# Kernel optimization log

Measured on AMD Instinct MI355X. Metric: run time of the kernel, lower is better.

The kernel has to match this reference:

```python
import jax, jax.numpy as jnp
import numpy as np

VOCAB = 50257
H = 1024
T = 4096


def setup_inputs() -> dict:
    key = jax.random.key(0)
    ks = jax.random.split(key, 6)
    scale = 1.0 / np.sqrt(H)  # matches torch LSTM uniform(-1/sqrt(H), 1/sqrt(H)) scale
    return {
        "tokens": jax.random.randint(ks[0], (T,), 0, VOCAB),
        "emb": jax.random.normal(ks[1], (VOCAB, H), dtype=jnp.float32) * 0.02,
        "w_ih": jax.random.uniform(ks[2], (4 * H, H), jnp.float32, -scale, scale),
        "w_hh": jax.random.uniform(ks[3], (4 * H, H), jnp.float32, -scale, scale),
        "b_ih": jax.random.uniform(ks[4], (4 * H,), jnp.float32, -scale, scale),
        "b_hh": jax.random.uniform(ks[5], (4 * H,), jnp.float32, -scale, scale),
    }


def _lstm(x, w_ih, w_hh, b_ih, b_hh):
    # x: [T, H]. Precompute input-side gate projections for all timesteps.
    gx = x @ w_ih.T + (b_ih + b_hh)  # [T, 4H]

    def step(carry, g_t):
        h, c = carry  # [H], [H]
        gates = g_t + h @ w_hh.T  # [4H]
        i, f, g, o = jnp.split(gates, 4)  # torch gate order: input, forget, cell, output
        i = jax.nn.sigmoid(i)
        f = jax.nn.sigmoid(f)
        g = jnp.tanh(g)
        o = jax.nn.sigmoid(o)
        c = f * c + i * g
        h = o * jnp.tanh(c)
        return (h, c), h

    h0 = jnp.zeros((H,), x.dtype)
    c0 = jnp.zeros((H,), x.dtype)
    (h_f, c_f), hs = jax.lax.scan(step, (h0, c0), gx)
    return hs, h_f, c_f  # hs: [T, H]


def reference(tokens, emb, w_ih, w_hh, b_ih, b_hh):
    x = emb[tokens]  # [T, H] embedding lookup
    hs, h_f, c_f = _lstm(x, w_ih, w_hh, b_ih, b_hh)
    output = hs[None, :, :]          # [1, T, H]  (batch_first, batch=1)
    h_n = h_f[None, None, :]         # [1, 1, H]
    c_n = c_f[None, None, :]         # [1, 1, H]
    return (output, (h_n, c_n))
```

## Files before the change

### kernel.cpp

```cpp
#include <hip/hip_runtime.h>
#include <hip/hip_bf16.h>

#define HD   1024
#define GD   4096
#define TT   4096
#define NWG  256

#define BM 128
#define BN 128
#define BK 16
#define LDP 132

__global__ __launch_bounds__(256, 2) void gemm_gx(
    const int* __restrict__ tokens,
    const float* __restrict__ emb,
    const float* __restrict__ Wih,
    const float* __restrict__ bih,
    const float* __restrict__ bhh,
    float* __restrict__ gxout)
{
    __shared__ float As[BK][LDP];
    __shared__ float Bs[BK][LDP];
    const int tid = threadIdx.x;
    const int m0 = blockIdx.x * BM;
    const int n0 = blockIdx.y * BN;
    const int tx = tid & 15;
    const int ty = tid >> 4;

    const int quad = tid & 3;
    const int r0   = tid >> 2;
    const int tok0 = tokens[m0 + r0];
    const int tok1 = tokens[m0 + r0 + 64];

    float acc[8][8] = {};

    for (int kt = 0; kt < HD; kt += BK) {
        float4 av0 = *reinterpret_cast<const float4*>(
            &emb[(size_t)tok0 * HD + kt + quad * 4]);
        float4 bv0 = *reinterpret_cast<const float4*>(
            &Wih[(size_t)(n0 + r0) * HD + kt + quad * 4]);
        float4 av1 = *reinterpret_cast<const float4*>(
            &emb[(size_t)tok1 * HD + kt + quad * 4]);
        float4 bv1 = *reinterpret_cast<const float4*>(
            &Wih[(size_t)(n0 + r0 + 64) * HD + kt + quad * 4]);
        As[quad * 4 + 0][r0] = av0.x;
        As[quad * 4 + 1][r0] = av0.y;
        As[quad * 4 + 2][r0] = av0.z;
        As[quad * 4 + 3][r0] = av0.w;
        Bs[quad * 4 + 0][r0] = bv0.x;
        Bs[quad * 4 + 1][r0] = bv0.y;
        Bs[quad * 4 + 2][r0] = bv0.z;
        Bs[quad * 4 + 3][r0] = bv0.w;
        As[quad * 4 + 0][r0 + 64] = av1.x;
        As[quad * 4 + 1][r0 + 64] = av1.y;
        As[quad * 4 + 2][r0 + 64] = av1.z;
        As[quad * 4 + 3][r0 + 64] = av1.w;
        Bs[quad * 4 + 0][r0 + 64] = bv1.x;
        Bs[quad * 4 + 1][r0 + 64] = bv1.y;
        Bs[quad * 4 + 2][r0 + 64] = bv1.z;
        Bs[quad * 4 + 3][r0 + 64] = bv1.w;
        __syncthreads();
#pragma unroll
        for (int k = 0; k < BK; ++k) {
            float4 a0 = *reinterpret_cast<const float4*>(&As[k][ty * 8]);
            float4 a1 = *reinterpret_cast<const float4*>(&As[k][ty * 8 + 4]);
            float4 b0 = *reinterpret_cast<const float4*>(&Bs[k][tx * 8]);
            float4 b1 = *reinterpret_cast<const float4*>(&Bs[k][tx * 8 + 4]);
            float a[8] = {a0.x, a0.y, a0.z, a0.w, a1.x, a1.y, a1.z, a1.w};
            float b[8] = {b0.x, b0.y, b0.z, b0.w, b1.x, b1.y, b1.z, b1.w};
#pragma unroll
            for (int i = 0; i < 8; ++i)
#pragma unroll
                for (int j = 0; j < 8; ++j)
                    acc[i][j] += a[i] * b[j];
        }
        __syncthreads();
    }

    float bias[8];
#pragma unroll
    for (int j = 0; j < 8; ++j) {
        int n = n0 + tx * 8 + j;
        bias[j] = bih[n] + bhh[n];
    }
#pragma unroll
    for (int i = 0; i < 8; ++i) {
        size_t o = (size_t)(m0 + ty * 8 + i) * GD + n0 + tx * 8;
        float4 s0 = {acc[i][0] + bias[0], acc[i][1] + bias[1],
                     acc[i][2] + bias[2], acc[i][3] + bias[3]};
        float4 s1 = {acc[i][4] + bias[4], acc[i][5] + bias[5],
                     acc[i][6] + bias[6], acc[i][7] + bias[7]};
        *reinterpret_cast<float4*>(&gxout[o]) = s0;
        *reinterpret_cast<float4*>(&gxout[o + 4]) = s1;
    }
}

__device__ __forceinline__ float sigmoid_(float x) {
    return 1.f / (1.f + __expf(-x));
}
__device__ __forceinline__ float tanh_(float x) {
    return __builtin_fmaf(2.f, 1.f / (1.f + __expf(-2.f * x)), -1.f);
}
__device__ __forceinline__ float bcast_(float v, int l) {
    return __uint_as_float(__builtin_amdgcn_readlane(__float_as_uint(v), l));
}
__device__ __forceinline__ void lds_barrier_() {
    asm volatile("s_waitcnt lgkmcnt(0)" ::: "memory");
    __builtin_amdgcn_s_barrier();
}

using u32x4 = __attribute__((ext_vector_type(4))) unsigned int;

__global__ __launch_bounds__(256, 1) void lstm_scan(
    const float* __restrict__ gx,
    const float* __restrict__ whh,
    float* __restrict__ out,
    unsigned long long* __restrict__ hbuf)
{
    const int tid   = threadIdx.x;
    const int b     = blockIdx.x;
    const int lane  = tid & 63;
    const int wv    = tid >> 6;
    const int chunk = lane & 15;
    const int gate  = lane >> 4;
    const int j     = b * 4 + wv;
    const int R     = gate * HD + j;

    float w[64];
    {
        const float* wrow = whh + (size_t)R * HD;
#pragma unroll
        for (int q = 0; q < 16; ++q) {
            float4 v = *reinterpret_cast<const float4*>(&wrow[chunk * 4 + q * 64]);
            w[q * 4 + 0] = v.x; w[q * 4 + 1] = v.y;
            w[q * 4 + 2] = v.z; w[q * 4 + 3] = v.w;
        }
    }

    __shared__ float h_lds[2][HD];
#pragma unroll
    for (int q = 0; q < 4; ++q) h_lds[0][tid * 4 + q] = 0.f;
    lds_barrier_();

    float c_reg = 0.f;
    float gx_cur = gx[R];

    const int tp = (tid + b) & 255;
    unsigned long long* const pb0 = hbuf + (size_t)tp * 4;
    unsigned long long* const pb1 = hbuf + HD + (size_t)tp * 4;

    for (int s = 1; s <= TT; ++s) {
        const int cb = (s - 1) & 1;
        const int nb = s & 1;

        float gx_nxt = 0.f;
        if (s < TT) gx_nxt = gx[(size_t)s * GD + R];

        float A0 = (chunk == 0) ? gx_cur : 0.f;
        float A1 = 0.f, A2 = 0.f, A3 = 0.f;
        {
            const float* hb = h_lds[cb];
#pragma unroll
            for (int q = 0; q < 4; ++q) {
                float4 h0 = *reinterpret_cast<const float4*>(&hb[chunk * 4 + (4 * q + 0) * 64]);
                float4 h1 = *reinterpret_cast<const float4*>(&hb[chunk * 4 + (4 * q + 1) * 64]);
                float4 h2 = *reinterpret_cast<const float4*>(&hb[chunk * 4 + (4 * q + 2) * 64]);
                float4 h3 = *reinterpret_cast<const float4*>(&hb[chunk * 4 + (4 * q + 3) * 64]);
                A0 = __builtin_fmaf(w[(4 * q + 0) * 4 + 0], h0.x, A0);
                A0 = __builtin_fmaf(w[(4 * q + 0) * 4 + 1], h0.y, A0);
                A0 = __builtin_fmaf(w[(4 * q + 0) * 4 + 2], h0.z, A0);
                A0 = __builtin_fmaf(w[(4 * q + 0) * 4 + 3], h0.w, A0);
                A1 = __builtin_fmaf(w[(4 * q + 1) * 4 + 0], h1.x, A1);
                A1 = __builtin_fmaf(w[(4 * q + 1) * 4 + 1], h1.y, A1);
                A1 = __builtin_fmaf(w[(4 * q + 1) * 4 + 2], h1.z, A1);
                A1 = __builtin_fmaf(w[(4 * q + 1) * 4 + 3], h1.w, A1);
                A2 = __builtin_fmaf(w[(4 * q + 2) * 4 + 0], h2.x, A2);
                A2 = __builtin_fmaf(w[(4 * q + 2) * 4 + 1], h2.y, A2);
                A2 = __builtin_fmaf(w[(4 * q + 2) * 4 + 2], h2.z, A2);
                A2 = __builtin_fmaf(w[(4 * q + 2) * 4 + 3], h2.w, A2);
                A3 = __builtin_fmaf(w[(4 * q + 3) * 4 + 0], h3.x, A3);
                A3 = __builtin_fmaf(w[(4 * q + 3) * 4 + 1], h3.y, A3);
                A3 = __builtin_fmaf(w[(4 * q + 3) * 4 + 2], h3.z, A3);
                A3 = __builtin_fmaf(w[(4 * q + 3) * 4 + 3], h3.w, A3);
            }
        }
        float acc = (A0 + A1) + (A2 + A3);
        acc += __shfl_xor(acc, 1, 64);
        acc += __shfl_xor(acc, 2, 64);
        acc += __shfl_xor(acc, 4, 64);
        acc += __shfl_xor(acc, 8, 64);
        float si = bcast_(acc, 0);
        float sf = bcast_(acc, 16);
        float sg = bcast_(acc, 32);
        float so = bcast_(acc, 48);

        float ii = sigmoid_(si);
        float ff = sigmoid_(sf);
        float gg = tanh_(sg);
        float oo = sigmoid_(so);
        c_reg = __builtin_fmaf(ff, c_reg, ii * gg);
        float hh = oo * tanh_(c_reg);

        if (s < TT) {
            if (lane == 0) {
                unsigned long long pkt =
                    ((unsigned long long)(unsigned)s << 32) | __float_as_uint(hh);
                __hip_atomic_store(&hbuf[(size_t)nb * HD + j], pkt,
                                   __ATOMIC_RELAXED, __HIP_MEMORY_SCOPE_AGENT);
            }
            gx_cur = gx_nxt;

            if (tid != 0) {
                const unsigned int us = (unsigned int)s;
                unsigned long long* src = nb ? pb1 : pb0;
                u32x4 q0, q1;
                int r = 0;
                for (;;) {
                    asm volatile(
                        "global_load_dwordx4 %0, %2, off sc1\n\t"
                        "global_load_dwordx4 %1, %2, off offset:16 sc1\n\t"
                        "s_waitcnt vmcnt(0)"
                        : "=v"(q0), "=v"(q1)
                        : "v"(src)
                        : "memory");
                    bool ok = (q0.y == us) & (q0.w == us) &
                              (q1.y == us) & (q1.w == us);
                    if (ok) break;
                    ++r;
                    if (r > (1 << 17)) break;
                    if (r >= 6) __builtin_amdgcn_s_sleep(1);
                }
                float4 hv;
                hv.x = __uint_as_float(q0.x);
                hv.y = __uint_as_float(q0.z);
                hv.z = __uint_as_float(q1.x);
                hv.w = __uint_as_float(q1.z);
                *reinterpret_cast<float4*>(&h_lds[nb][tp * 4]) = hv;
            }
            if (lane == 0) {
                h_lds[nb][j] = hh;
                out[(size_t)(s - 1) * HD + j] = hh;
            }
            lds_barrier_();
        } else {
            if (lane == 0) {
                out[(size_t)(s - 1) * HD + j] = hh;
                out[(size_t)TT * HD + j] = hh;
                out[(size_t)TT * HD + HD + j] = c_reg;
            }
        }
    }
}

extern "C" void kernel_launch(void* const* d_in, const int* in_sizes, int n_in,
                              void* d_out, int out_size, void* d_ws, size_t ws_size,
                              hipStream_t stream) {
    const int*   tokens = (const int*)d_in[0];
    const float* emb    = (const float*)d_in[1];
    const float* w_ih   = (const float*)d_in[2];
    const float* w_hh   = (const float*)d_in[3];
    const float* b_ih   = (const float*)d_in[4];
    const float* b_hh   = (const float*)d_in[5];
    float* out = (float*)d_out;

    char* ws = (char*)d_ws;
    const size_t HBUF_BYTES = (size_t)2 * HD * 8;
    unsigned long long* hbuf = (unsigned long long*)ws;
    float* gx = (float*)(ws + 65536);

    hipMemsetAsync(hbuf, 0, HBUF_BYTES, stream);
    gemm_gx<<<dim3(TT / BM, GD / BN), 256, 0, stream>>>(tokens, emb, w_ih,
                                                        b_ih, b_hh, gx);
    lstm_scan<<<NWG, 256, 0, stream>>>(gx, w_hh, out, hbuf);
}
```

Measured before the change: 18.78 ms.

## Replicate LSTM scan per XCD with XCD-local mailboxes for h exchange

```diff
diff --git a/kernel.cpp b/kernel.cpp
--- a/kernel.cpp
+++ b/kernel.cpp
@@ -5,6 +5,8 @@
 #define GD   4096
 #define TT   4096
 #define NWG  256
+
+using u32x4 = __attribute__((ext_vector_type(4))) unsigned int;
 
 #define BM 128
 #define BN 128
@@ -101,154 +103,209 @@
 __device__ __forceinline__ float tanh_(float x) {
     return __builtin_fmaf(2.f, 1.f / (1.f + __expf(-2.f * x)), -1.f);
 }
-__device__ __forceinline__ float bcast_(float v, int l) {
-    return __uint_as_float(__builtin_amdgcn_readlane(__float_as_uint(v), l));
-}
 __device__ __forceinline__ void lds_barrier_() {
     asm volatile("s_waitcnt lgkmcnt(0)" ::: "memory");
     __builtin_amdgcn_s_barrier();
 }
-
-using u32x4 = __attribute__((ext_vector_type(4))) unsigned int;
-
-__global__ __launch_bounds__(256, 1) void lstm_scan(
+__device__ __forceinline__ float rl_(float v, int l) {
+    return __uint_as_float(__builtin_amdgcn_readlane(__float_as_uint(v), l));
+}
+__device__ __forceinline__ float dot4_(float4 a, float4 b, float c) {
+    c = __builtin_fmaf(a.x, b.x, c);
+    c = __builtin_fmaf(a.y, b.y, c);
+    c = __builtin_fmaf(a.z, b.z, c);
+    return __builtin_fmaf(a.w, b.w, c);
+}
+
+__global__ __launch_bounds__(512, 1) void lstm_scan(
     const float* __restrict__ gx,
     const float* __restrict__ whh,
     float* __restrict__ out,
-    unsigned long long* __restrict__ hbuf)
+    unsigned long long* __restrict__ mbF,
+    unsigned long long* __restrict__ mbS,
+    int* __restrict__ ctr)
 {
-    const int tid   = threadIdx.x;
-    const int b     = blockIdx.x;
-    const int lane  = tid & 63;
-    const int wv    = tid >> 6;
+    const int tid  = threadIdx.x;
+    const int lane = tid & 63;
+    const int wv   = tid >> 6;
+    const int sub  = lane >> 4;
     const int chunk = lane & 15;
-    const int gate  = lane >> 4;
-    const int j     = b * 4 + wv;
-    const int R     = gate * HD + j;
-
-    float w[64];
-    {
-        const float* wrow = whh + (size_t)R * HD;
-#pragma unroll
-        for (int q = 0; q < 16; ++q) {
-            float4 v = *reinterpret_cast<const float4*>(&wrow[chunk * 4 + q * 64]);
-            w[q * 4 + 0] = v.x; w[q * 4 + 1] = v.y;
-            w[q * 4 + 2] = v.z; w[q * 4 + 3] = v.w;
-        }
-    }
-
+
+    __shared__ int s_role, s_xcd, s_fail;
+    __shared__ float wlds[8][16][256];
     __shared__ float h_lds[2][HD];
-#pragma unroll
-    for (int q = 0; q < 4; ++q) h_lds[0][tid * 4 + q] = 0.f;
+
+    if (tid == 0) {
+        unsigned int x;
+        asm volatile("s_getreg_b32 %0, hwreg(20, 0, 32)" : "=s"(x));
+        x &= 7;
+        s_xcd  = (int)x;
+        s_role = atomicAdd(&ctr[x], 1);
+        s_fail = 0;
+    }
+    __syncthreads();
+    const int role = s_role;
+    if (role >= 32) return;
+
+    unsigned long long* const fastb = mbF + (size_t)s_xcd * 2048;
+    unsigned long long* const slowb = mbS + (size_t)s_xcd * 2048;
+    const int j0 = role * 32 + wv * 4;
+
+    float4 wreg[16][3];
+#pragma unroll
+    for (int rr = 0; rr < 16; ++rr) {
+        const float* wr = whh + (size_t)((rr >> 2) * HD + j0 + (rr & 3)) * HD;
+#pragma unroll
+        for (int q = 0; q < 3; ++q)
+            wreg[rr][q] = *reinterpret_cast<const float4*>(&wr[4 * lane + 256 * q]);
+        *reinterpret_cast<float4*>(&wlds[wv][rr][4 * lane]) =
+            *reinterpret_cast<const float4*>(&wr[4 * lane + 768]);
+    }
+
+    *reinterpret_cast<float2*>(&h_lds[0][2 * tid]) = float2{0.f, 0.f};
     lds_barrier_();
 
-    float c_reg = 0.f;
-    float gx_cur = gx[R];
-
-    const int tp = (tid + b) & 255;
-    unsigned long long* const pb0 = hbuf + (size_t)tp * 4;
-    unsigned long long* const pb1 = hbuf + HD + (size_t)tp * 4;
+    const int grow = (lane >> 2) * HD + j0 + (lane & 3);
+    float gxc = (lane < 16) ? gx[grow] : 0.f;
+
+    float cst[4] = {0.f, 0.f, 0.f, 0.f};
+    bool slow = false;
+    const int e0 = 2 * tid;
 
     for (int s = 1; s <= TT; ++s) {
         const int cb = (s - 1) & 1;
         const int nb = s & 1;
 
-        float gx_nxt = 0.f;
-        if (s < TT) gx_nxt = gx[(size_t)s * GD + R];
-
-        float A0 = (chunk == 0) ? gx_cur : 0.f;
-        float A1 = 0.f, A2 = 0.f, A3 = 0.f;
+        float gxn = 0.f;
+        if (s < TT && lane < 16) gxn = gx[(size_t)s * GD + grow];
+
+        float4 hq0 = *reinterpret_cast<const float4*>(&h_lds[cb][4 * lane]);
+        float4 hq1 = *reinterpret_cast<const float4*>(&h_lds[cb][4 * lane + 256]);
+        float4 hq2 = *reinterpret_cast<const float4*>(&h_lds[cb][4 * lane + 512]);
+        float4 hq3 = *reinterpret_cast<const float4*>(&h_lds[cb][4 * lane + 768]);
+
+        float ii[4], hh[4];
         {
-            const float* hb = h_lds[cb];
-#pragma unroll
-            for (int q = 0; q < 4; ++q) {
-                float4 h0 = *reinterpret_cast<const float4*>(&hb[chunk * 4 + (4 * q + 0) * 64]);
-                float4 h1 = *reinterpret_cast<const float4*>(&hb[chunk * 4 + (4 * q + 1) * 64]);
-                float4 h2 = *reinterpret_cast<const float4*>(&hb[chunk * 4 + (4 * q + 2) * 64]);
-                float4 h3 = *reinterpret_cast<const float4*>(&hb[chunk * 4 + (4 * q + 3) * 64]);
-                A0 = __builtin_fmaf(w[(4 * q + 0) * 4 + 0], h0.x, A0);
-                A0 = __builtin_fmaf(w[(4 * q + 0) * 4 + 1], h0.y, A0);
-                A0 = __builtin_fmaf(w[(4 * q + 0) * 4 + 2], h0.z, A0);
-                A0 = __builtin_fmaf(w[(4 * q + 0) * 4 + 3], h0.w, A0);
-                A1 = __builtin_fmaf(w[(4 * q + 1) * 4 + 0], h1.x, A1);
-                A1 = __builtin_fmaf(w[(4 * q + 1) * 4 + 1], h1.y, A1);
-                A1 = __builtin_fmaf(w[(4 * q + 1) * 4 + 2], h1.z, A1);
-                A1 = __builtin_fmaf(w[(4 * q + 1) * 4 + 3], h1.w, A1);
-                A2 = __builtin_fmaf(w[(4 * q + 2) * 4 + 0], h2.x, A2);
-                A2 = __builtin_fmaf(w[(4 * q + 2) * 4 + 1], h2.y, A2);
-                A2 = __builtin_fmaf(w[(4 * q + 2) * 4 + 2], h2.z, A2);
-                A2 = __builtin_fmaf(w[(4 * q + 2) * 4 + 3], h2.w, A2);
-                A3 = __builtin_fmaf(w[(4 * q + 3) * 4 + 0], h3.x, A3);
-                A3 = __builtin_fmaf(w[(4 * q + 3) * 4 + 1], h3.y, A3);
-                A3 = __builtin_fmaf(w[(4 * q + 3) * 4 + 2], h3.z, A3);
-                A3 = __builtin_fmaf(w[(4 * q + 3) * 4 + 3], h3.w, A3);
-            }
-        }
-        float acc = (A0 + A1) + (A2 + A3);
-        acc += __shfl_xor(acc, 1, 64);
-        acc += __shfl_xor(acc, 2, 64);
-        acc += __shfl_xor(acc, 4, 64);
-        acc += __shfl_xor(acc, 8, 64);
-        float si = bcast_(acc, 0);
-        float sf = bcast_(acc, 16);
-        float sg = bcast_(acc, 32);
-        float so = bcast_(acc, 48);
-
-        float ii = sigmoid_(si);
-        float ff = sigmoid_(sf);
-        float gg = tanh_(sg);
-        float oo = sigmoid_(so);
-        c_reg = __builtin_fmaf(ff, c_reg, ii * gg);
-        float hh = oo * tanh_(c_reg);
-
-        if (s < TT) {
-            if (lane == 0) {
-                unsigned long long pkt =
-                    ((unsigned long long)(unsigned)s << 32) | __float_as_uint(hh);
-                __hip_atomic_store(&hbuf[(size_t)nb * HD + j], pkt,
-                                   __ATOMIC_RELAXED, __HIP_MEMORY_SCOPE_AGENT);
-            }
-            gx_cur = gx_nxt;
-
-            if (tid != 0) {
-                const unsigned int us = (unsigned int)s;
-                unsigned long long* src = nb ? pb1 : pb0;
-                u32x4 q0, q1;
+            float a8[8];
+#pragma unroll
+            for (int rr = 0; rr < 8; ++rr) {
+                float4 wl = *reinterpret_cast<const float4*>(&wlds[wv][rr][4 * lane]);
+                float a = dot4_(wreg[rr][0], hq0, 0.f);
+                a = dot4_(wreg[rr][1], hq1, a);
+                a = dot4_(wreg[rr][2], hq2, a);
+                a8[rr] = dot4_(wl, hq3, a);
+            }
+#pragma unroll
+            for (int rr = 0; rr < 8; ++rr) {
+                a8[rr] += __shfl_xor(a8[rr], 1, 64);
+                a8[rr] += __shfl_xor(a8[rr], 2, 64);
+                a8[rr] += __shfl_xor(a8[rr], 4, 64);
+                a8[rr] += __shfl_xor(a8[rr], 8, 64);
+            }
+#pragma unroll
+            for (int m = 0; m < 4; ++m) {
+                float pi = rl_(a8[m], 0) + rl_(a8[m], 16) +
+                           rl_(a8[m], 32) + rl_(a8[m], 48) + rl_(gxc, m);
+                float pf = rl_(a8[4 + m], 0) + rl_(a8[4 + m], 16) +
+                           rl_(a8[4 + m], 32) + rl_(a8[4 + m], 48) + rl_(gxc, 4 + m);
+                ii[m] = sigmoid_(pi);
+                cst[m] *= sigmoid_(pf);
+            }
+        }
+        {
+            float a8[8];
+#pragma unroll
+            for (int rr = 0; rr < 8; ++rr) {
+                float4 wl = *reinterpret_cast<const float4*>(&wlds[wv][8 + rr][4 * lane]);
+                float a = dot4_(wreg[8 + rr][0], hq0, 0.f);
+                a = dot4_(wreg[8 + rr][1], hq1, a);
+                a = dot4_(wreg[8 + rr][2], hq2, a);
+                a8[rr] = dot4_(wl, hq3, a);
+            }
+#pragma unroll
+            for (int rr = 0; rr < 8; ++rr) {
+                a8[rr] += __shfl_xor(a8[rr], 1, 64);
+                a8[rr] += __shfl_xor(a8[rr], 2, 64);
+                a8[rr] += __shfl_xor(a8[rr], 4, 64);
+                a8[rr] += __shfl_xor(a8[rr], 8, 64);
+            }
+#pragma unroll
+            for (int m = 0; m < 4; ++m) {
+                float pg = rl_(a8[m], 0) + rl_(a8[m], 16) +
+                           rl_(a8[m], 32) + rl_(a8[m], 48) + rl_(gxc, 8 + m);
+                float po = rl_(a8[4 + m], 0) + rl_(a8[4 + m], 16) +
+                           rl_(a8[4 + m], 32) + rl_(a8[4 + m], 48) + rl_(gxc, 12 + m);
+                cst[m] = __builtin_fmaf(ii[m], tanh_(pg), cst[m]);
+                hh[m] = sigmoid_(po) * tanh_(cst[m]);
+            }
+        }
+        gxc = gxn;
+
+        float hpub = (sub == 0) ? hh[0] : (sub == 1) ? hh[1]
+                   : (sub == 2) ? hh[2] : hh[3];
+
+        if (s == TT) {
+            if (chunk == 0) {
+                float cpub = (sub == 0) ? cst[0] : (sub == 1) ? cst[1]
+                           : (sub == 2) ? cst[2] : cst[3];
+                out[(size_t)(s - 1) * HD + j0 + sub] = hpub;
+                out[(size_t)TT * HD + j0 + sub] = hpub;
+                out[(size_t)TT * HD + HD + j0 + sub] = cpub;
+            }
+            break;
+        }
+
+        const unsigned int us = (unsigned int)s;
+        if (chunk == 0) {
+            unsigned long long pkt =
+                ((unsigned long long)us << 32) | __float_as_uint(hpub);
+            __hip_atomic_store(&fastb[(size_t)nb * HD + j0 + sub], pkt,
+                               __ATOMIC_RELAXED, __HIP_MEMORY_SCOPE_WORKGROUP);
+            __hip_atomic_store(&slowb[(size_t)nb * HD + j0 + sub], pkt,
+                               __ATOMIC_RELAXED, __HIP_MEMORY_SCOPE_AGENT);
+            out[(size_t)(s - 1) * HD + j0 + sub] = hpub;
+        }
+
+        {
+            u32x4 q;
+            bool ok = false;
+            if (!slow) {
+                const unsigned long long* pf = fastb + (size_t)nb * HD + e0;
+                for (int r = 0; r < 48 && !ok; ++r) {
+                    asm volatile(
+                        "global_load_dwordx4 %0, %1, off sc0\n\t"
+                        "s_waitcnt vmcnt(0)"
+                        : "=v"(q) : "v"(pf) : "memory");
+                    ok = (q.y == us) & (q.w == us);
+                }
+                if (!ok) slow = true;
+            }
+            if (!ok) {
+                const unsigned long long* ps = slowb + (size_t)nb * HD + e0;
                 int r = 0;
                 for (;;) {
-                    asm volatile(
-                        "global_load_dwordx4 %0, %2, off sc1\n\t"
-                        "global_load_dwordx4 %1, %2, off offset:16 sc1\n\t"
-                        "s_waitcnt vmcnt(0)"
-                        : "=v"(q0), "=v"(q1)
-                        : "v"(src)
-                        : "memory");
-                    bool ok = (q0.y == us) & (q0.w == us) &
-                              (q1.y == us) & (q1.w == us);
-                    if (ok) break;
+                    unsigned long long v0 = __hip_atomic_load(
+                        &ps[0], __ATOMIC_RELAXED, __HIP_MEMORY_SCOPE_AGENT);
+                    unsigned long long v1 = __hip_atomic_load(
+                        &ps[1], __ATOMIC_RELAXED, __HIP_MEMORY_SCOPE_AGENT);
+                    if (((unsigned int)(v0 >> 32) == us) &
+                        ((unsigned int)(v1 >> 32) == us)) {
+                        q.x = (unsigned int)v0;
+                        q.z = (unsigned int)v1;
+                        ok = true;
+                        break;
+                    }
                     ++r;
-                    if (r > (1 << 17)) break;
-                    if (r >= 6) __builtin_amdgcn_s_sleep(1);
+                    if (r > 8) __builtin_amdgcn_s_sleep(2);
+                    if (r > 32768) break;
                 }
-                float4 hv;
-                hv.x = __uint_as_float(q0.x);
-                hv.y = __uint_as_float(q0.z);
-                hv.z = __uint_as_float(q1.x);
-                hv.w = __uint_as_float(q1.z);
-                *reinterpret_cast<float4*>(&h_lds[nb][tp * 4]) = hv;
-            }
-            if (lane == 0) {
-                h_lds[nb][j] = hh;
-                out[(size_t)(s - 1) * HD + j] = hh;
-            }
-            lds_barrier_();
-        } else {
-            if (lane == 0) {
-                out[(size_t)(s - 1) * HD + j] = hh;
-                out[(size_t)TT * HD + j] = hh;
-                out[(size_t)TT * HD + HD + j] = c_reg;
-            }
-        }
+                if (!ok) s_fail = 1;
+            }
+            *reinterpret_cast<float2*>(&h_lds[nb][e0]) =
+                float2{__uint_as_float(q.x), __uint_as_float(q.z)};
+        }
+        lds_barrier_();
+        if (s_fail) return;
     }
 }
 
@@ -264,12 +321,13 @@
     float* out = (float*)d_out;
 
     char* ws = (char*)d_ws;
-    const size_t HBUF_BYTES = (size_t)2 * HD * 8;
-    unsigned long long* hbuf = (unsigned long long*)ws;
-    float* gx = (float*)(ws + 65536);
-
-    hipMemsetAsync(hbuf, 0, HBUF_BYTES, stream);
+    unsigned long long* mbF = (unsigned long long*)ws;
+    unsigned long long* mbS = (unsigned long long*)(ws + 131072);
+    int* ctr = (int*)(ws + 262144);
+    float* gxbuf = (float*)(ws + (1 << 20));
+
+    (void)hipMemsetAsync(ws, 0, 262144 + 4096, stream);
     gemm_gx<<<dim3(TT / BM, GD / BN), 256, 0, stream>>>(tokens, emb, w_ih,
-                                                        b_ih, b_hh, gx);
-    lstm_scan<<<NWG, 256, 0, stream>>>(gx, w_hh, out, hbuf);
-}
+                                                        b_ih, b_hh, gxbuf);
+    lstm_scan<<<NWG, 512, 0, stream>>>(gxbuf, w_hh, out, mbF, mbS, ctr);
+}
```

Result: slower. 25.74 ms (+37.0%).
